# Kernel optimization log

Hardware: AMD Instinct MI355X
Metric: run time of the kernel (lower is better)

## Reference

```python
import jax, jax.numpy as jnp
import numpy as np

B, T_PH, H = 32, 512, 256
N_BINS = 256
DUR_MAX = 8
MAX_LEN = T_PH * DUR_MAX  # 4096


def setup_inputs() -> dict:
    key = jax.random.key(0)
    k = jax.random.split(key, 6)
    x = jax.random.normal(k[0], (B, T_PH, H), dtype=jnp.float32)
    pitch_target = jax.random.normal(k[1], (B, T_PH), dtype=jnp.float32)
    energy_target = jax.random.normal(k[2], (B, T_PH), dtype=jnp.float32)
    duration = jax.random.randint(k[3], (B, T_PH), 0, DUR_MAX).astype(jnp.int32)
    # sorted bin boundaries (linear quantization, as in pitch_quantization='linear')
    pitch_bins = jnp.linspace(-3.0, 3.0, N_BINS - 1, dtype=jnp.float32)
    energy_bins = jnp.linspace(-3.0, 3.0, N_BINS - 1, dtype=jnp.float32)
    pitch_emb = jax.random.normal(k[4], (N_BINS, H), dtype=jnp.float32) * 0.02
    energy_emb = jax.random.normal(k[5], (N_BINS, H), dtype=jnp.float32) * 0.02
    return {
        "x": x,
        "pitch_target": pitch_target,
        "energy_target": energy_target,
        "pitch_bins": pitch_bins,
        "energy_bins": energy_bins,
        "pitch_emb": pitch_emb,
        "energy_emb": energy_emb,
        "duration": duration,
        "max_len": MAX_LEN,
    }


def reference(x, pitch_target, energy_target, pitch_bins, energy_bins,
              pitch_emb, energy_emb, duration, max_len):
    # --- phoneme-level pitch/energy: bucketize + embedding lookup, add to x ---
    # torch.bucketize(v, bins) (right=False) == searchsorted(bins, v, side='left')
    p_idx = jnp.searchsorted(pitch_bins, pitch_target)      # [B, T_ph] int
    x = x + pitch_emb[p_idx]                                 # gather [B, T_ph, H]
    e_idx = jnp.searchsorted(energy_bins, energy_target)
    x = x + energy_emb[e_idx]

    # --- LengthRegulator: expand phoneme i duration[b,i] times, pad to max_len ---
    dur = duration.astype(jnp.int32)
    csum = jnp.cumsum(dur, axis=1)                           # [B, T_ph]
    mel_len = csum[:, -1]                                    # [B]
    t = jnp.arange(max_len, dtype=jnp.int32)                 # [M]
    # frame t belongs to phoneme idx where csum[idx-1] <= t < csum[idx]
    ph_idx = jax.vmap(lambda c: jnp.searchsorted(c, t, side='right'))(csum)  # [B, M]
    ph_idx = jnp.minimum(ph_idx, dur.shape[1] - 1)
    out = jnp.take_along_axis(x, ph_idx[:, :, None], axis=1)  # [B, M, H]
    valid = (t[None, :] < mel_len[:, None])                   # [B, M] (padding)
    out = jnp.where(valid[:, :, None], out, 0.0)
    return out, mel_len
```

## Files before the change

kernel.cpp:

```cpp
#include <hip/hip_runtime.h>

#define B_SZ 32
#define T_PH 512
#define H_DIM 256
#define N_EDGES 255
#define MAX_LEN 4096

__global__ void prep_kernel(const int* __restrict__ dur,
                            const float* __restrict__ pt,
                            const float* __restrict__ et,
                            const float* __restrict__ pbins,
                            const float* __restrict__ ebins,
                            int* __restrict__ pack_idx,
                            int* __restrict__ ph_idx,
                            float* __restrict__ mel_out) {
    const int b = blockIdx.x;
    const int tid = threadIdx.x;
    __shared__ int s[T_PH];
    __shared__ float pb[N_EDGES];
    __shared__ float eb[N_EDGES];

    if (tid < N_EDGES) pb[tid] = pbins[tid];
    else if (tid >= 256 && tid < 256 + N_EDGES) eb[tid - 256] = ebins[tid - 256];

    const int d = dur[b * T_PH + tid];
    s[tid] = d;
    __syncthreads();
#pragma unroll
    for (int off = 1; off < T_PH; off <<= 1) {
        int v = (tid >= off) ? s[tid - off] : 0;
        __syncthreads();
        s[tid] += v;
        __syncthreads();
    }
    const int end   = s[tid];
    const int start = end - d;
    const int mel   = s[T_PH - 1];

    const float pv = pt[b * T_PH + tid];
    const float ev = et[b * T_PH + tid];
    int lo = 0, hi = N_EDGES;
    while (lo < hi) { int m = (lo + hi) >> 1; if (pb[m] < pv) lo = m + 1; else hi = m; }
    const int pi = lo;
    lo = 0; hi = N_EDGES;
    while (lo < hi) { int m = (lo + hi) >> 1; if (eb[m] < ev) lo = m + 1; else hi = m; }
    const int ei = lo;
    pack_idx[b * T_PH + tid] = pi | (ei << 16);

    int* pr = ph_idx + (size_t)b * MAX_LEN;
    for (int t = start; t < end; ++t) pr[t] = tid;
    for (int t = mel + tid; t < MAX_LEN; t += T_PH) pr[t] = -1;

    if (tid == T_PH - 1) mel_out[b] = (float)mel;
}

__global__ void expand_kernel(const float* __restrict__ x,
                              const float* __restrict__ pemb,
                              const float* __restrict__ eemb,
                              const int* __restrict__ pack_idx,
                              const int* __restrict__ ph_idx,
                              float* __restrict__ out) {
    const int sub   = threadIdx.x >> 6;
    const int lane4 = threadIdx.x & 63;
    const int frame = blockIdx.x * 4 + sub;
    const int b = frame >> 12;

    const int ph = ph_idx[frame];
    float4 val = make_float4(0.f, 0.f, 0.f, 0.f);
    if (ph >= 0) {
        const int pk = pack_idx[b * T_PH + ph];
        const int pi = pk & 0xffff;
        const int ei = pk >> 16;
        const float4* xr = (const float4*)(x + (size_t)(b * T_PH + ph) * H_DIM);
        const float4* pr = (const float4*)(pemb + (size_t)pi * H_DIM);
        const float4* er = (const float4*)(eemb + (size_t)ei * H_DIM);
        const float4 a = xr[lane4];
        const float4 p = pr[lane4];
        const float4 e = er[lane4];
        val.x = a.x + p.x + e.x;
        val.y = a.y + p.y + e.y;
        val.z = a.z + p.z + e.z;
        val.w = a.w + p.w + e.w;
    }
    ((float4*)out)[(size_t)frame * 64 + lane4] = val;
}

extern "C" void kernel_launch(void* const* d_in, const int* in_sizes, int n_in,
                              void* d_out, int out_size, void* d_ws, size_t ws_size,
                              hipStream_t stream) {
    const float* x     = (const float*)d_in[0];
    const float* pt    = (const float*)d_in[1];
    const float* et    = (const float*)d_in[2];
    const float* pbins = (const float*)d_in[3];
    const float* ebins = (const float*)d_in[4];
    const float* pemb  = (const float*)d_in[5];
    const float* eemb  = (const float*)d_in[6];
    const int*   dur   = (const int*)d_in[7];

    float* out = (float*)d_out;
    float* mel_out = out + (size_t)B_SZ * MAX_LEN * H_DIM;

    int* pack_idx = (int*)d_ws;
    int* ph_idx   = pack_idx + B_SZ * T_PH;

    prep_kernel<<<B_SZ, T_PH, 0, stream>>>(dur, pt, et, pbins, ebins,
                                           pack_idx, ph_idx, mel_out);

    const int frames = B_SZ * MAX_LEN;
    expand_kernel<<<frames / 4, 256, 0, stream>>>(x, pemb, eemb,
                                                  pack_idx, ph_idx, out);
}
```

Baseline: 34.51 us.

## Pack per-frame indices in prep, coalesce frame writes, use nontemporal output stores

The prep kernel now builds a per-frame packed word holding the phoneme, pitch bin and energy bin. Each thread binary-searches the cumsum for its 8-frame chunk and writes it as int4 vectors, replacing the old scattered per-phoneme loop writes and the separate pad fill. The expand kernel reads one packed word instead of a dependent second lookup, and writes output with nontemporal stores to avoid polluting cache with the 128MB result. The risk is that nontemporal stores may behave differently on MI355X.

```diff
diff --git a/kernel.cpp b/kernel.cpp
--- a/kernel.cpp
+++ b/kernel.cpp
@@ -6,17 +6,19 @@
 #define N_EDGES 255
 #define MAX_LEN 4096
 
+typedef float f32x4 __attribute__((ext_vector_type(4)));
+
 __global__ void prep_kernel(const int* __restrict__ dur,
                             const float* __restrict__ pt,
                             const float* __restrict__ et,
                             const float* __restrict__ pbins,
                             const float* __restrict__ ebins,
-                            int* __restrict__ pack_idx,
-                            int* __restrict__ ph_idx,
+                            int* __restrict__ frames,
                             float* __restrict__ mel_out) {
     const int b = blockIdx.x;
     const int tid = threadIdx.x;
-    __shared__ int s[T_PH];
+    __shared__ int cs[T_PH];
+    __shared__ int packv[T_PH];
     __shared__ float pb[N_EDGES];
     __shared__ float eb[N_EDGES];
 
@@ -24,18 +26,15 @@
     else if (tid >= 256 && tid < 256 + N_EDGES) eb[tid - 256] = ebins[tid - 256];
 
     const int d = dur[b * T_PH + tid];
-    s[tid] = d;
+    cs[tid] = d;
     __syncthreads();
 #pragma unroll
     for (int off = 1; off < T_PH; off <<= 1) {
-        int v = (tid >= off) ? s[tid - off] : 0;
+        int v = (tid >= off) ? cs[tid - off] : 0;
         __syncthreads();
-        s[tid] += v;
+        cs[tid] += v;
         __syncthreads();
     }
-    const int end   = s[tid];
-    const int start = end - d;
-    const int mel   = s[T_PH - 1];
 
     const float pv = pt[b * T_PH + tid];
     const float ev = et[b * T_PH + tid];
@@ -45,11 +44,32 @@
     lo = 0; hi = N_EDGES;
     while (lo < hi) { int m = (lo + hi) >> 1; if (eb[m] < ev) lo = m + 1; else hi = m; }
     const int ei = lo;
-    pack_idx[b * T_PH + tid] = pi | (ei << 16);
+    packv[tid] = tid | (pi << 9) | (ei << 17);
+    __syncthreads();
 
-    int* pr = ph_idx + (size_t)b * MAX_LEN;
-    for (int t = start; t < end; ++t) pr[t] = tid;
-    for (int t = mel + tid; t < MAX_LEN; t += T_PH) pr[t] = -1;
+    const int mel = cs[T_PH - 1];
+
+    const int t0 = tid * 8;
+    int p = 0;
+    if (t0 < mel) {
+        int l = 0, h = T_PH;
+        while (l < h) { int m = (l + h) >> 1; if (cs[m] > t0) h = m; else l = m + 1; }
+        p = l;
+    }
+    int o[8];
+#pragma unroll
+    for (int j = 0; j < 8; ++j) {
+        const int t = t0 + j;
+        int v = -1;
+        if (t < mel) {
+            while (cs[p] <= t) ++p;
+            v = packv[p];
+        }
+        o[j] = v;
+    }
+    int4* fr = (int4*)(frames + (size_t)b * MAX_LEN);
+    fr[tid * 2]     = make_int4(o[0], o[1], o[2], o[3]);
+    fr[tid * 2 + 1] = make_int4(o[4], o[5], o[6], o[7]);
 
     if (tid == T_PH - 1) mel_out[b] = (float)mel;
 }
@@ -57,32 +77,28 @@
 __global__ void expand_kernel(const float* __restrict__ x,
                               const float* __restrict__ pemb,
                               const float* __restrict__ eemb,
-                              const int* __restrict__ pack_idx,
-                              const int* __restrict__ ph_idx,
+                              const int* __restrict__ frames,
                               float* __restrict__ out) {
     const int sub   = threadIdx.x >> 6;
     const int lane4 = threadIdx.x & 63;
     const int frame = blockIdx.x * 4 + sub;
     const int b = frame >> 12;
 
-    const int ph = ph_idx[frame];
-    float4 val = make_float4(0.f, 0.f, 0.f, 0.f);
-    if (ph >= 0) {
-        const int pk = pack_idx[b * T_PH + ph];
-        const int pi = pk & 0xffff;
-        const int ei = pk >> 16;
-        const float4* xr = (const float4*)(x + (size_t)(b * T_PH + ph) * H_DIM);
-        const float4* pr = (const float4*)(pemb + (size_t)pi * H_DIM);
-        const float4* er = (const float4*)(eemb + (size_t)ei * H_DIM);
-        const float4 a = xr[lane4];
-        const float4 p = pr[lane4];
-        const float4 e = er[lane4];
-        val.x = a.x + p.x + e.x;
-        val.y = a.y + p.y + e.y;
-        val.z = a.z + p.z + e.z;
-        val.w = a.w + p.w + e.w;
+    const int pk = frames[frame];
+    f32x4 val = {0.f, 0.f, 0.f, 0.f};
+    if (pk >= 0) {
+        const int ph = pk & 511;
+        const int pi = (pk >> 9) & 255;
+        const int ei = (pk >> 17) & 255;
+        const f32x4* xr = (const f32x4*)(x + (size_t)(b * T_PH + ph) * H_DIM);
+        const f32x4* pr = (const f32x4*)(pemb + (size_t)pi * H_DIM);
+        const f32x4* er = (const f32x4*)(eemb + (size_t)ei * H_DIM);
+        const f32x4 a = xr[lane4];
+        const f32x4 p = pr[lane4];
+        const f32x4 e = er[lane4];
+        val = a + p + e;
     }
-    ((float4*)out)[(size_t)frame * 64 + lane4] = val;
+    __builtin_nontemporal_store(val, (f32x4*)out + (size_t)frame * 64 + lane4);
 }
 
 extern "C" void kernel_launch(void* const* d_in, const int* in_sizes, int n_in,
@@ -100,13 +116,11 @@
     float* out = (float*)d_out;
     float* mel_out = out + (size_t)B_SZ * MAX_LEN * H_DIM;
 
-    int* pack_idx = (int*)d_ws;
-    int* ph_idx   = pack_idx + B_SZ * T_PH;
+    int* frames = (int*)d_ws;
 
     prep_kernel<<<B_SZ, T_PH, 0, stream>>>(dur, pt, et, pbins, ebins,
-                                           pack_idx, ph_idx, mel_out);
+                                           frames, mel_out);
 
-    const int frames = B_SZ * MAX_LEN;
-    expand_kernel<<<frames / 4, 256, 0, stream>>>(x, pemb, eemb,
-                                                  pack_idx, ph_idx, out);
+    const int nframes = B_SZ * MAX_LEN;
+    expand_kernel<<<nframes / 4, 256, 0, stream>>>(x, pemb, eemb, frames, out);
 }
```

Measured after the change: 33.18 us. 3.9% less time.
